# Optimization experiments

Hardware: AMD Instinct MI355X
Metric: run time of the kernel (lower is better)

## Reference

```python
import jax, jax.numpy as jnp
import numpy as np

B, S, D = 8, 1024, 1024
H, DK = 16, 64  # num_heads, d_k; H*DK == D
NEG_INF = 1e29


def setup_inputs() -> dict:
    key = jax.random.key(0)
    ks = jax.random.split(key, 12)
    sc = 1.0 / np.sqrt(D)
    q = jax.random.normal(ks[0], (B, S, D), jnp.float32)
    k = jax.random.normal(ks[1], (B, S, D), jnp.float32)
    v = jax.random.normal(ks[2], (B, S, D), jnp.float32)
    # causal mask, broadcast per batch (mask==0 positions are masked out)
    mask = jnp.broadcast_to(jnp.tril(jnp.ones((S, S), jnp.int32)), (B, S, S))
    Wq = jax.random.normal(ks[3], (D, D), jnp.float32) * sc
    bq = jax.random.normal(ks[4], (D,), jnp.float32) * 0.01
    Wk = jax.random.normal(ks[5], (D, D), jnp.float32) * sc
    bk = jax.random.normal(ks[6], (D,), jnp.float32) * 0.01
    Wv = jax.random.normal(ks[7], (D, D), jnp.float32) * sc
    bv = jax.random.normal(ks[8], (D,), jnp.float32) * 0.01
    Wo = jax.random.normal(ks[9], (D, D), jnp.float32) * sc
    bo = jax.random.normal(ks[10], (D,), jnp.float32) * 0.01
    return {"q": q, "k": k, "v": v, "mask": mask,
            "Wq": Wq, "bq": bq, "Wk": Wk, "bk": bk,
            "Wv": Wv, "bv": bv, "Wo": Wo, "bo": bo}


def reference(q, k, v, mask, Wq, bq, Wk, bk, Wv, bv, Wo, bo):
    # Linear projections (torch Linear: x @ W.T + b)
    q1 = q @ Wq.T + bq
    k1 = k @ Wk.T + bk
    v1 = v @ Wv.T + bv
    # [B, S, D] -> [B, H, S, DK]
    def split_heads(x):
        return x.reshape(B, S, H, DK).transpose(0, 2, 1, 3)
    q3, k3, v3 = split_heads(q1), split_heads(k1), split_heads(v1)
    # scores [B, H, S, S]
    scores = jnp.einsum('bhqd,bhkd->bhqk', q3, k3) / jnp.sqrt(jnp.float32(DK))
    scores = jnp.where(mask[:, None, :, :] == 0, -NEG_INF, scores)
    probs = jax.nn.softmax(scores, axis=-1)
    attn = jnp.einsum('bhqk,bhkd->bhqd', probs, v3)  # [B, H, S, DK]
    out = attn.transpose(0, 2, 1, 3).reshape(B, S, D)
    return out @ Wo.T + bo
```

## Files before the change

kernel.cpp:

```cpp
#include <hip/hip_runtime.h>
#include <hip/hip_bf16.h>
#include <stdint.h>

constexpr int NB = 8;
constexpr int NS = 1024;
constexpr int ND = 1024;
constexpr int NH = 16;
constexpr int NDK = 64;
constexpr int NT = NS / 64;

typedef __bf16 bf16_t;
typedef __attribute__((ext_vector_type(8))) __bf16 bf16x8;
typedef __attribute__((ext_vector_type(4))) __bf16 bf16x4;
typedef __attribute__((ext_vector_type(4))) float f32x4;

#define GLL16(g, s) __builtin_amdgcn_global_load_lds( \
    (const __attribute__((address_space(1))) void*)(g), \
    (__attribute__((address_space(3))) void*)(s), 16, 0, 0)

__device__ __forceinline__ void cvt_body(const float* __restrict__ s,
                                         bf16_t* __restrict__ d, long n) {
  long i0 = (long)(blockIdx.x * blockDim.x + threadIdx.x) * 4;
  long step = (long)gridDim.x * blockDim.x * 4;
  for (long i = i0; i < n; i += step) {
    float4 f = *(const float4*)(s + i);
    bf16x4 o;
    o[0] = (bf16_t)f.x; o[1] = (bf16_t)f.y; o[2] = (bf16_t)f.z; o[3] = (bf16_t)f.w;
    *(bf16x4*)(d + i) = o;
  }
}

__global__ __launch_bounds__(256) void cvt3_kernel(const float* s0, bf16_t* d0,
                                                   const float* s1, bf16_t* d1,
                                                   const float* s2, bf16_t* d2, long n) {
  const float* s = blockIdx.y == 0 ? s0 : blockIdx.y == 1 ? s1 : s2;
  bf16_t* d = blockIdx.y == 0 ? d0 : blockIdx.y == 1 ? d1 : d2;
  cvt_body(s, d, n);
}

__global__ __launch_bounds__(256) void cvt4_kernel(const float* s0, bf16_t* d0,
                                                   const float* s1, bf16_t* d1,
                                                   const float* s2, bf16_t* d2,
                                                   const float* s3, bf16_t* d3, long n) {
  const float* s = blockIdx.y == 0 ? s0 : blockIdx.y == 1 ? s1 : blockIdx.y == 2 ? s2 : s3;
  bf16_t* d = blockIdx.y == 0 ? d0 : blockIdx.y == 1 ? d1 : blockIdx.y == 2 ? d2 : d3;
  cvt_body(s, d, n);
}

template<bool OUT_F32>
__device__ __forceinline__ void gemm_body(bf16_t* S,
                                          const bf16_t* __restrict__ A,
                                          const bf16_t* __restrict__ W,
                                          const float* __restrict__ bias,
                                          void* __restrict__ Cout,
                                          int M, int N, int K, int bx, int by) {
  const int tid = threadIdx.x;
  const int l = tid & 63, w = tid >> 6;
  const int wr = w >> 1, wc = w & 1;
  const int g = l >> 4, r = l & 15;
  const int m0 = by * 256, n0 = bx * 128;
  const int wbase = w * 512;

  auto stageA2 = [&](int q, int t, int half) {
#pragma unroll
    for (int it = half * 2; it < half * 2 + 2; ++it) {
      int idx = it * 512 + tid;
      int row = idx >> 3, c = (idx & 7) ^ (row & 7);
      GLL16(A + (size_t)(m0 + row) * K + (t << 6) + c * 8,
            S + q * 24576 + it * 4096 + wbase);
    }
  };
  auto stageB2 = [&](int q, int t) {
#pragma unroll
    for (int it = 0; it < 2; ++it) {
      int idx = it * 512 + tid;
      int row = idx >> 3, c = (idx & 7) ^ (row & 7);
      GLL16(W + (size_t)(n0 + row) * K + (t << 6) + c * 8,
            S + q * 24576 + 16384 + it * 4096 + wbase);
    }
  };

  f32x4 acc[4][4] = {};
  const int NKT = K >> 6;

  stageA2(0, 0, 0); stageA2(0, 0, 1); stageB2(0, 0);
  stageA2(1, 1, 0); stageA2(1, 1, 1); stageB2(1, 1);

  int q = 0;
  for (int t = 0; t < NKT; ++t) {
    const bool pf = (t + 2 < NKT);
    int q2 = q + 2; if (q2 >= 3) q2 -= 3;

    if (t + 1 < NKT) asm volatile("s_waitcnt vmcnt(6)" ::: "memory");
    else             asm volatile("s_waitcnt vmcnt(0)" ::: "memory");
    __builtin_amdgcn_s_barrier();

    const bf16_t* a_ = S + q * 24576;
    const bf16_t* b_ = a_ + 16384;

#pragma unroll
    for (int kk = 0; kk < 2; ++kk) {
      bf16x8 bw[4];
#pragma unroll
      for (int n = 0; n < 4; ++n) {
        int row = wc * 64 + n * 16 + r;
        bw[n] = *(const bf16x8*)(b_ + row * 64 + (((kk * 4 + g) ^ (row & 7)) << 3));
      }
#pragma unroll
      for (int mh = 0; mh < 2; ++mh) {
        bf16x8 af[2];
#pragma unroll
        for (int i = 0; i < 2; ++i) {
          int row = wr * 64 + (mh * 2 + i) * 16 + r;
          af[i] = *(const bf16x8*)(a_ + row * 64 + (((kk * 4 + g) ^ (row & 7)) << 3));
        }
        if (pf) {
          int ph = kk * 2 + mh;
          if (ph == 0)      stageA2(q2, t + 2, 0);
          else if (ph == 1) stageA2(q2, t + 2, 1);
          else if (ph == 2) stageB2(q2, t + 2);
        }
        __builtin_amdgcn_s_barrier();
        asm volatile("s_waitcnt lgkmcnt(0)" ::: "memory");
        __builtin_amdgcn_sched_barrier(0);
        __builtin_amdgcn_s_setprio(1);
#pragma unroll
        for (int i = 0; i < 2; ++i)
#pragma unroll
          for (int n = 0; n < 4; ++n)
            acc[mh * 2 + i][n] = __builtin_amdgcn_mfma_f32_16x16x32_bf16(
                af[i], bw[n], acc[mh * 2 + i][n], 0, 0, 0);
        __builtin_amdgcn_s_setprio(0);
        __builtin_amdgcn_sched_barrier(0);
      }
    }
    ++q; if (q >= 3) q -= 3;
  }

#pragma unroll
  for (int n = 0; n < 4; ++n) {
    int col = n0 + wc * 64 + n * 16 + r;
    float bv = bias[col];
#pragma unroll
    for (int m = 0; m < 4; ++m) {
      int row0 = m0 + wr * 64 + m * 16 + g * 4;
#pragma unroll
      for (int j = 0; j < 4; ++j) {
        float vv = acc[m][n][j] + bv;
        if (OUT_F32)
          ((float*)Cout)[(size_t)(row0 + j) * N + col] = vv;
        else
          ((bf16_t*)Cout)[(size_t)(row0 + j) * N + col] = (bf16_t)vv;
      }
    }
  }
}

__global__ __launch_bounds__(512, 2) void gemm_bt(const bf16_t* __restrict__ A,
                                                  const bf16_t* __restrict__ W,
                                                  const float* __restrict__ bias,
                                                  float* __restrict__ Cout,
                                                  int M, int N, int K) {
  __shared__ bf16_t S[3 * 24576];
  const int o = blockIdx.x;
  const int xcd = o & 7, s = o >> 3;
  const int bx = s & 7, u = s >> 3;
  const int by = xcd + 8 * u;
  gemm_body<true>(S, A, W, bias, (void*)Cout, M, N, K, bx, by);
}

__global__ __launch_bounds__(512, 2) void gemm_qkv(
    const bf16_t* A0, const bf16_t* W0, const float* b0, bf16_t* C0,
    const bf16_t* A1, const bf16_t* W1, const float* b1, bf16_t* C1,
    const bf16_t* A2, const bf16_t* W2, const float* b2, bf16_t* C2,
    int M, int N, int K) {
  __shared__ bf16_t S[3 * 24576];
  const int o = blockIdx.x;
  const int xcd = o & 7, s = o >> 3;
  const int bx = s & 7, u = s >> 3;
  const int zby = xcd + 8 * u;
  const int z = zby >> 5, by = zby & 31;
  const bf16_t* A = z == 0 ? A0 : z == 1 ? A1 : A2;
  const bf16_t* W = z == 0 ? W0 : z == 1 ? W1 : W2;
  const float* bb = z == 0 ? b0 : z == 1 ? b1 : b2;
  bf16_t* C = z == 0 ? C0 : z == 1 ? C1 : C2;
  gemm_body<false>(S, A, W, bb, (void*)C, M, N, K, bx, by);
}

__global__ __launch_bounds__(256, 4) void attn_kernel(const bf16_t* __restrict__ Q1,
                                                      const bf16_t* __restrict__ K1,
                                                      const bf16_t* __restrict__ V1,
                                                      bf16_t* __restrict__ attn) {
  __shared__ bf16_t Kt[2][64 * 64];
  __shared__ bf16_t Vt[2][64 * 64];
  __shared__ bf16_t Pl[4][16 * 64];

  const int tid = threadIdx.x;
  const int l = tid & 63, w = tid >> 6;
  const int g = l >> 4, r = l & 15;

  const int o = blockIdx.x;
  const int os = (o & 7) * 128 + (o >> 3);
  const int pair = os & 7, hb = os >> 3;
  const int h = hb & 15, b = hb >> 4;

  constexpr float SC = 0.18033688011112042f;

  for (int ph = 0; ph < 2; ++ph) {
    const int qt = ph ? (NT - 1 - pair) : pair;
    const int qrow_g = qt * 64 + w * 16 + r;

    const bf16_t* qptr = Q1 + ((size_t)b * NS + qrow_g) * ND + h * 64;
    bf16x8 qf0 = *(const bf16x8*)(qptr + g * 8);
    bf16x8 qf1 = *(const bf16x8*)(qptr + 32 + g * 8);
#pragma unroll
    for (int i = 0; i < 8; ++i) {
      qf0[i] = (bf16_t)((float)qf0[i] * SC);
      qf1[i] = (bf16_t)((float)qf1[i] * SC);
    }

    float mrun = -1e30f, lrun = 0.f;
    f32x4 oacc[4] = {};

    __syncthreads();

    bf16x8 vr0, vr1;
    {
#pragma unroll
      for (int it = 0; it < 2; ++it) {
        int idx = it * 256 + tid;
        int key = idx >> 3;
        int dkg = ((idx & 7) ^ (key & 7)) << 3;
        GLL16(K1 + ((size_t)b * NS + key) * ND + h * 64 + dkg,
              &Kt[0][(it * 256 + w * 64) * 8]);
      }
      vr0 = *(const bf16x8*)(V1 + ((size_t)b * NS + l) * ND + h * 64 + w * 8);
      vr1 = *(const bf16x8*)(V1 + ((size_t)b * NS + l) * ND + h * 64 + (4 + w) * 8);
    }

    for (int kt = 0; kt <= qt; ++kt) {
      const int p = kt & 1;
      const int k0 = kt * 64;

#pragma unroll
      for (int it = 0; it < 2; ++it) {
        int dkb = (it * 4 + w) * 8;
#pragma unroll
        for (int jj = 0; jj < 8; ++jj) {
          int dk = dkb + jj;
          int boff = dk * 128 + ((l * 2) ^ ((dk & 7) << 4));
          *(bf16_t*)((char*)Vt[p] + boff) = (it ? vr1 : vr0)[jj];
        }
      }
      __syncthreads();

      if (kt < qt) {
        const int k0n = k0 + 64;
#pragma unroll
        for (int it = 0; it < 2; ++it) {
          int idx = it * 256 + tid;
          int key = idx >> 3;
          int dkg = ((idx & 7) ^ (key & 7)) << 3;
          GLL16(K1 + ((size_t)b * NS + k0n + key) * ND + h * 64 + dkg,
                &Kt[p ^ 1][(it * 256 + w * 64) * 8]);
        }
        vr0 = *(const bf16x8*)(V1 + ((size_t)b * NS + k0n + l) * ND + h * 64 + w * 8);
        vr1 = *(const bf16x8*)(V1 + ((size_t)b * NS + k0n + l) * ND + h * 64 + (4 + w) * 8);
      }

      f32x4 sacc[4] = {};
      __builtin_amdgcn_s_setprio(1);
#pragma unroll
      for (int n = 0; n < 4; ++n) {
        int key = n * 16 + r;
#pragma unroll
        for (int kk = 0; kk < 2; ++kk) {
          int dk2 = kk * 32 + g * 8;
          int boff = key * 128 + ((dk2 * 2) ^ ((key & 7) << 4));
          bf16x8 kf = *(const bf16x8*)((char*)Kt[p] + boff);
          sacc[n] = __builtin_amdgcn_mfma_f32_16x16x32_bf16(kf, kk == 0 ? qf0 : qf1, sacc[n], 0, 0, 0);
        }
      }
      __builtin_amdgcn_s_setprio(0);

      if (kt == qt) {
#pragma unroll
        for (int n = 0; n < 4; ++n)
#pragma unroll
          for (int j = 0; j < 4; ++j)
            if (k0 + n * 16 + g * 4 + j > qrow_g) sacc[n][j] = -1e30f;
      }

      float mx;
      {
        float t0 = fmaxf(fmaxf(sacc[0][0], sacc[0][1]), fmaxf(sacc[0][2], sacc[0][3]));
        float t1 = fmaxf(fmaxf(sacc[1][0], sacc[1][1]), fmaxf(sacc[1][2], sacc[1][3]));
        float t2 = fmaxf(fmaxf(sacc[2][0], sacc[2][1]), fmaxf(sacc[2][2], sacc[2][3]));
        float t3 = fmaxf(fmaxf(sacc[3][0], sacc[3][1]), fmaxf(sacc[3][2], sacc[3][3]));
        mx = fmaxf(fmaxf(t0, t1), fmaxf(t2, t3));
      }
      mx = fmaxf(mx, __shfl_xor(mx, 16));
      mx = fmaxf(mx, __shfl_xor(mx, 32));

      if (!__all(mx <= mrun + 8.0f)) {
        float m_new = fmaxf(mrun, mx);
        float esc = __builtin_amdgcn_exp2f(mrun - m_new);
        mrun = m_new;
        lrun *= esc;
#pragma unroll
        for (int n = 0; n < 4; ++n)
#pragma unroll
          for (int j = 0; j < 4; ++j) oacc[n][j] *= esc;
      }

      float rsum = 0.f;
#pragma unroll
      for (int n = 0; n < 4; ++n) {
        bf16x4 p4;
#pragma unroll
        for (int j = 0; j < 4; ++j) {
          float pe = __builtin_amdgcn_exp2f(sacc[n][j] - mrun);
          rsum += pe;
          p4[j] = (bf16_t)pe;
        }
        *(bf16x4*)((char*)Pl[w] + r * 128 + ((n * 32 + g * 8) ^ ((r & 7) << 4))) = p4;
      }
      rsum += __shfl_xor(rsum, 16);
      rsum += __shfl_xor(rsum, 32);
      lrun += rsum;

      __builtin_amdgcn_s_setprio(1);
#pragma unroll
      for (int kk = 0; kk < 2; ++kk) {
        bf16x8 pf = *(const bf16x8*)((char*)Pl[w] + r * 128 + ((kk * 64 + g * 16) ^ ((r & 7) << 4)));
#pragma unroll
        for (int n = 0; n < 4; ++n) {
          int dkr = n * 16 + r;
          bf16x8 vf = *(const bf16x8*)((char*)Vt[p] + dkr * 128 + ((kk * 64 + g * 16) ^ ((r & 7) << 4)));
          oacc[n] = __builtin_amdgcn_mfma_f32_16x16x32_bf16(vf, pf, oacc[n], 0, 0, 0);
        }
      }
      __builtin_amdgcn_s_setprio(0);
    }

    float linv = 1.0f / lrun;
#pragma unroll
    for (int n = 0; n < 4; ++n) {
      bf16x4 o4;
#pragma unroll
      for (int j = 0; j < 4; ++j) o4[j] = (bf16_t)(oacc[n][j] * linv);
      *(bf16x4*)(attn + ((size_t)b * NS + qrow_g) * ND + h * 64 + n * 16 + g * 4) = o4;
    }
  }
}

extern "C" void kernel_launch(void* const* d_in, const int* in_sizes, int n_in,
                              void* d_out, int out_size, void* d_ws, size_t ws_size,
                              hipStream_t stream) {
  const float* q  = (const float*)d_in[0];
  const float* k  = (const float*)d_in[1];
  const float* v  = (const float*)d_in[2];
  const float* Wq = (const float*)d_in[4];
  const float* bq = (const float*)d_in[5];
  const float* Wk = (const float*)d_in[6];
  const float* bk = (const float*)d_in[7];
  const float* Wv = (const float*)d_in[8];
  const float* bv = (const float*)d_in[9];
  const float* Wo = (const float*)d_in[10];
  const float* bo = (const float*)d_in[11];
  float* out = (float*)d_out;

  const size_t NX = (size_t)NB * NS * ND;
  const size_t NW = (size_t)ND * ND;
  char* ws = (char*)d_ws;
  size_t off = 0;
  auto alloc = [&](size_t bytes) {
    char* p = ws + off;
    off += (bytes + 255) & ~(size_t)255;
    return p;
  };
  bf16_t* xq  = (bf16_t*)alloc(NX * 2);
  bf16_t* xk  = (bf16_t*)alloc(NX * 2);
  bf16_t* xv  = (bf16_t*)alloc(NX * 2);
  bf16_t* wqb = (bf16_t*)alloc(NW * 2);
  bf16_t* wkb = (bf16_t*)alloc(NW * 2);
  bf16_t* wvb = (bf16_t*)alloc(NW * 2);
  bf16_t* wob = (bf16_t*)alloc(NW * 2);
  bf16_t* q1  = (bf16_t*)alloc(NX * 2);
  bf16_t* k1  = (bf16_t*)alloc(NX * 2);
  bf16_t* v1  = (bf16_t*)alloc(NX * 2);
  bf16_t* at  = xq;

  dim3 blk(256);
  cvt3_kernel<<<dim3(1024, 3), blk, 0, stream>>>(q, xq, k, xk, v, xv, (long)NX);
  cvt4_kernel<<<dim3(128, 4), blk, 0, stream>>>(Wq, wqb, Wk, wkb, Wv, wvb, Wo, wob, (long)NW);

  gemm_qkv<<<dim3(768), dim3(512), 0, stream>>>(
      xq, wqb, bq, q1, xk, wkb, bk, k1, xv, wvb, bv, v1, NB * NS, ND, ND);

  attn_kernel<<<dim3((NT / 2) * NH * NB), blk, 0, stream>>>(q1, k1, v1, at);

  gemm_bt<<<dim3(256), dim3(512), 0, stream>>>(at, wob, bo, out, NB * NS, ND, ND);
}
```

Measured before the change: 158.3 us.

## Fuse fp32-to-bf16 activation conversion into the QKV projection GEMM

Removes the separate cvt3 kernel that turned q/k/v into bf16 in a workspace buffer. The QKV GEMM now reads fp32 activations straight into registers, converts them to bf16 and writes them into a double-buffered swizzled LDS tile, while weights still use async global-to-LDS loads in a triple buffer. This avoids writing and rereading about 48MB of bf16 activations and one kernel launch. In exchange the A-tile loads go through registers, which costs register pressure and VGPR-mediated LDS writes, and the pipeline now has a single barrier per k-step.

```diff
diff --git a/kernel.cpp b/kernel.cpp
--- a/kernel.cpp
+++ b/kernel.cpp
@@ -8,6 +8,7 @@
 constexpr int NH = 16;
 constexpr int NDK = 64;
 constexpr int NT = NS / 64;
+constexpr int NKT = ND / 64;
 
 typedef __bf16 bf16_t;
 typedef __attribute__((ext_vector_type(8))) __bf16 bf16x8;
@@ -30,14 +31,6 @@
   }
 }
 
-__global__ __launch_bounds__(256) void cvt3_kernel(const float* s0, bf16_t* d0,
-                                                   const float* s1, bf16_t* d1,
-                                                   const float* s2, bf16_t* d2, long n) {
-  const float* s = blockIdx.y == 0 ? s0 : blockIdx.y == 1 ? s1 : s2;
-  bf16_t* d = blockIdx.y == 0 ? d0 : blockIdx.y == 1 ? d1 : d2;
-  cvt_body(s, d, n);
-}
-
 __global__ __launch_bounds__(256) void cvt4_kernel(const float* s0, bf16_t* d0,
                                                    const float* s1, bf16_t* d1,
                                                    const float* s2, bf16_t* d2,
@@ -47,13 +40,21 @@
   cvt_body(s, d, n);
 }
 
-template<bool OUT_F32>
-__device__ __forceinline__ void gemm_body(bf16_t* S,
-                                          const bf16_t* __restrict__ A,
-                                          const bf16_t* __restrict__ W,
-                                          const float* __restrict__ bias,
-                                          void* __restrict__ Cout,
-                                          int M, int N, int K, int bx, int by) {
+__global__ __launch_bounds__(512, 2) void gemm_qkv(
+    const float* A0, const bf16_t* W0, const float* b0, bf16_t* C0,
+    const float* A1, const bf16_t* W1, const float* b1, bf16_t* C1,
+    const float* A2, const bf16_t* W2, const float* b2, bf16_t* C2) {
+  __shared__ bf16_t S[2 * 16384 + 3 * 8192];
+  const int o = blockIdx.x;
+  const int xcd = o & 7, s = o >> 3;
+  const int bx = s & 7, u = s >> 3;
+  const int zby = xcd + 8 * u;
+  const int z = zby >> 5, by = zby & 31;
+  const float* A = z == 0 ? A0 : z == 1 ? A1 : A2;
+  const bf16_t* W = z == 0 ? W0 : z == 1 ? W1 : W2;
+  const float* bb = z == 0 ? b0 : z == 1 ? b1 : b2;
+  bf16_t* C = z == 0 ? C0 : z == 1 ? C1 : C2;
+
   const int tid = threadIdx.x;
   const int l = tid & 63, w = tid >> 6;
   const int wr = w >> 1, wc = w & 1;
@@ -61,97 +62,101 @@
   const int m0 = by * 256, n0 = bx * 128;
   const int wbase = w * 512;
 
-  auto stageA2 = [&](int q, int t, int half) {
-#pragma unroll
-    for (int it = half * 2; it < half * 2 + 2; ++it) {
-      int idx = it * 512 + tid;
-      int row = idx >> 3, c = (idx & 7) ^ (row & 7);
-      GLL16(A + (size_t)(m0 + row) * K + (t << 6) + c * 8,
-            S + q * 24576 + it * 4096 + wbase);
-    }
-  };
-  auto stageB2 = [&](int q, int t) {
+  bf16_t* Ab = S;
+  bf16_t* Bb = S + 32768;
+
+  float4 fa[8];
+  auto issueA = [&](int t) {
+#pragma unroll
+    for (int it = 0; it < 4; ++it) {
+      const float* p = A + (size_t)(m0 + it * 64 + (tid >> 3)) * ND + t * 64 + (tid & 7) * 8;
+      fa[it * 2]     = *(const float4*)p;
+      fa[it * 2 + 1] = *(const float4*)(p + 4);
+    }
+  };
+  auto writeA = [&](int ab) {
+#pragma unroll
+    for (int it = 0; it < 4; ++it) {
+      int row = it * 64 + (tid >> 3), c = tid & 7;
+      bf16x8 ov;
+      ov[0] = (bf16_t)fa[it * 2].x;     ov[1] = (bf16_t)fa[it * 2].y;
+      ov[2] = (bf16_t)fa[it * 2].z;     ov[3] = (bf16_t)fa[it * 2].w;
+      ov[4] = (bf16_t)fa[it * 2 + 1].x; ov[5] = (bf16_t)fa[it * 2 + 1].y;
+      ov[6] = (bf16_t)fa[it * 2 + 1].z; ov[7] = (bf16_t)fa[it * 2 + 1].w;
+      *(bf16x8*)(Ab + ab * 16384 + row * 64 + ((c ^ (row & 7)) << 3)) = ov;
+    }
+  };
+  auto stageB = [&](int qb, int t) {
 #pragma unroll
     for (int it = 0; it < 2; ++it) {
       int idx = it * 512 + tid;
       int row = idx >> 3, c = (idx & 7) ^ (row & 7);
-      GLL16(W + (size_t)(n0 + row) * K + (t << 6) + c * 8,
-            S + q * 24576 + 16384 + it * 4096 + wbase);
+      GLL16(W + (size_t)(n0 + row) * ND + (t << 6) + c * 8,
+            Bb + qb * 8192 + it * 4096 + wbase);
     }
   };
 
   f32x4 acc[4][4] = {};
-  const int NKT = K >> 6;
-
-  stageA2(0, 0, 0); stageA2(0, 0, 1); stageB2(0, 0);
-  stageA2(1, 1, 0); stageA2(1, 1, 1); stageB2(1, 1);
-
-  int q = 0;
+
+  issueA(0);
+  stageB(0, 0);
+  stageB(1, 1);
+  asm volatile("s_waitcnt vmcnt(0)" ::: "memory");
+  __builtin_amdgcn_sched_barrier(0);
+  writeA(0);
+  asm volatile("s_waitcnt lgkmcnt(0)" ::: "memory");
+  __builtin_amdgcn_s_barrier();
+
   for (int t = 0; t < NKT; ++t) {
-    const bool pf = (t + 2 < NKT);
-    int q2 = q + 2; if (q2 >= 3) q2 -= 3;
-
-    if (t + 1 < NKT) asm volatile("s_waitcnt vmcnt(6)" ::: "memory");
-    else             asm volatile("s_waitcnt vmcnt(0)" ::: "memory");
-    __builtin_amdgcn_s_barrier();
-
-    const bf16_t* a_ = S + q * 24576;
-    const bf16_t* b_ = a_ + 16384;
-
+    if (t + 1 < NKT) issueA(t + 1);
+    __builtin_amdgcn_sched_barrier(0);
+    if (t + 2 < NKT) stageB((t + 2) % 3, t + 2);
+    __builtin_amdgcn_sched_barrier(0);
+
+    const bf16_t* a_ = Ab + (t & 1) * 16384;
+    const bf16_t* b_ = Bb + (t % 3) * 8192;
 #pragma unroll
     for (int kk = 0; kk < 2; ++kk) {
-      bf16x8 bw[4];
+      bf16x8 af[4], bw[4];
+#pragma unroll
+      for (int m = 0; m < 4; ++m) {
+        int row = wr * 64 + m * 16 + r;
+        af[m] = *(const bf16x8*)(a_ + row * 64 + (((kk * 4 + g) ^ (row & 7)) << 3));
+      }
 #pragma unroll
       for (int n = 0; n < 4; ++n) {
         int row = wc * 64 + n * 16 + r;
         bw[n] = *(const bf16x8*)(b_ + row * 64 + (((kk * 4 + g) ^ (row & 7)) << 3));
       }
-#pragma unroll
-      for (int mh = 0; mh < 2; ++mh) {
-        bf16x8 af[2];
-#pragma unroll
-        for (int i = 0; i < 2; ++i) {
-          int row = wr * 64 + (mh * 2 + i) * 16 + r;
-          af[i] = *(const bf16x8*)(a_ + row * 64 + (((kk * 4 + g) ^ (row & 7)) << 3));
-        }
-        if (pf) {
-          int ph = kk * 2 + mh;
-          if (ph == 0)      stageA2(q2, t + 2, 0);
-          else if (ph == 1) stageA2(q2, t + 2, 1);
-          else if (ph == 2) stageB2(q2, t + 2);
-        }
-        __builtin_amdgcn_s_barrier();
-        asm volatile("s_waitcnt lgkmcnt(0)" ::: "memory");
-        __builtin_amdgcn_sched_barrier(0);
-        __builtin_amdgcn_s_setprio(1);
-#pragma unroll
-        for (int i = 0; i < 2; ++i)
-#pragma unroll
-          for (int n = 0; n < 4; ++n)
-            acc[mh * 2 + i][n] = __builtin_amdgcn_mfma_f32_16x16x32_bf16(
-                af[i], bw[n], acc[mh * 2 + i][n], 0, 0, 0);
-        __builtin_amdgcn_s_setprio(0);
-        __builtin_amdgcn_sched_barrier(0);
-      }
-    }
-    ++q; if (q >= 3) q -= 3;
+      __builtin_amdgcn_s_setprio(1);
+#pragma unroll
+      for (int m = 0; m < 4; ++m)
+#pragma unroll
+        for (int n = 0; n < 4; ++n)
+          acc[m][n] = __builtin_amdgcn_mfma_f32_16x16x32_bf16(af[m], bw[n], acc[m][n], 0, 0, 0);
+      __builtin_amdgcn_s_setprio(0);
+    }
+
+    if (t + 1 < NKT) {
+      if (t + 2 < NKT) asm volatile("s_waitcnt vmcnt(2)" ::: "memory");
+      else             asm volatile("s_waitcnt vmcnt(0)" ::: "memory");
+      __builtin_amdgcn_sched_barrier(0);
+      writeA((t + 1) & 1);
+    }
+    asm volatile("s_waitcnt lgkmcnt(0)" ::: "memory");
+    __builtin_amdgcn_s_barrier();
   }
 
 #pragma unroll
   for (int n = 0; n < 4; ++n) {
     int col = n0 + wc * 64 + n * 16 + r;
-    float bv = bias[col];
+    float bv = bb[col];
 #pragma unroll
     for (int m = 0; m < 4; ++m) {
       int row0 = m0 + wr * 64 + m * 16 + g * 4;
 #pragma unroll
-      for (int j = 0; j < 4; ++j) {
-        float vv = acc[m][n][j] + bv;
-        if (OUT_F32)
-          ((float*)Cout)[(size_t)(row0 + j) * N + col] = vv;
-        else
-          ((bf16_t*)Cout)[(size_t)(row0 + j) * N + col] = (bf16_t)vv;
-      }
+      for (int j = 0; j < 4; ++j)
+        C[(size_t)(row0 + j) * ND + col] = (bf16_t)(acc[m][n][j] + bv);
     }
   }
 }
@@ -166,25 +171,102 @@
   const int xcd = o & 7, s = o >> 3;
   const int bx = s & 7, u = s >> 3;
   const int by = xcd + 8 * u;
-  gemm_body<true>(S, A, W, bias, (void*)Cout, M, N, K, bx, by);
-}
-
-__global__ __launch_bounds__(512, 2) void gemm_qkv(
-    const bf16_t* A0, const bf16_t* W0, const float* b0, bf16_t* C0,
-    const bf16_t* A1, const bf16_t* W1, const float* b1, bf16_t* C1,
-    const bf16_t* A2, const bf16_t* W2, const float* b2, bf16_t* C2,
-    int M, int N, int K) {
-  __shared__ bf16_t S[3 * 24576];
-  const int o = blockIdx.x;
-  const int xcd = o & 7, s = o >> 3;
-  const int bx = s & 7, u = s >> 3;
-  const int zby = xcd + 8 * u;
-  const int z = zby >> 5, by = zby & 31;
-  const bf16_t* A = z == 0 ? A0 : z == 1 ? A1 : A2;
-  const bf16_t* W = z == 0 ? W0 : z == 1 ? W1 : W2;
-  const float* bb = z == 0 ? b0 : z == 1 ? b1 : b2;
-  bf16_t* C = z == 0 ? C0 : z == 1 ? C1 : C2;
-  gemm_body<false>(S, A, W, bb, (void*)C, M, N, K, bx, by);
+
+  const int tid = threadIdx.x;
+  const int l = tid & 63, w = tid >> 6;
+  const int wr = w >> 1, wc = w & 1;
+  const int g = l >> 4, r = l & 15;
+  const int m0 = by * 256, n0 = bx * 128;
+  const int wbase = w * 512;
+
+  auto stageA2 = [&](int q, int t, int half) {
+#pragma unroll
+    for (int it = half * 2; it < half * 2 + 2; ++it) {
+      int idx = it * 512 + tid;
+      int row = idx >> 3, c = (idx & 7) ^ (row & 7);
+      GLL16(A + (size_t)(m0 + row) * K + (t << 6) + c * 8,
+            S + q * 24576 + it * 4096 + wbase);
+    }
+  };
+  auto stageB2 = [&](int q, int t) {
+#pragma unroll
+    for (int it = 0; it < 2; ++it) {
+      int idx = it * 512 + tid;
+      int row = idx >> 3, c = (idx & 7) ^ (row & 7);
+      GLL16(W + (size_t)(n0 + row) * K + (t << 6) + c * 8,
+            S + q * 24576 + 16384 + it * 4096 + wbase);
+    }
+  };
+
+  f32x4 acc[4][4] = {};
+  const int NKT2 = K >> 6;
+
+  stageA2(0, 0, 0); stageA2(0, 0, 1); stageB2(0, 0);
+  stageA2(1, 1, 0); stageA2(1, 1, 1); stageB2(1, 1);
+
+  int q = 0;
+  for (int t = 0; t < NKT2; ++t) {
+    const bool pf = (t + 2 < NKT2);
+    int q2 = q + 2; if (q2 >= 3) q2 -= 3;
+
+    if (t + 1 < NKT2) asm volatile("s_waitcnt vmcnt(6)" ::: "memory");
+    else              asm volatile("s_waitcnt vmcnt(0)" ::: "memory");
+    __builtin_amdgcn_s_barrier();
+
+    const bf16_t* a_ = S + q * 24576;
+    const bf16_t* b_ = a_ + 16384;
+
+#pragma unroll
+    for (int kk = 0; kk < 2; ++kk) {
+      bf16x8 bw[4];
+#pragma unroll
+      for (int n = 0; n < 4; ++n) {
+        int row = wc * 64 + n * 16 + r;
+        bw[n] = *(const bf16x8*)(b_ + row * 64 + (((kk * 4 + g) ^ (row & 7)) << 3));
+      }
+#pragma unroll
+      for (int mh = 0; mh < 2; ++mh) {
+        bf16x8 af[2];
+#pragma unroll
+        for (int i = 0; i < 2; ++i) {
+          int row = wr * 64 + (mh * 2 + i) * 16 + r;
+          af[i] = *(const bf16x8*)(a_ + row * 64 + (((kk * 4 + g) ^ (row & 7)) << 3));
+        }
+        if (pf) {
+          int ph = kk * 2 + mh;
+          if (ph == 0)      stageA2(q2, t + 2, 0);
+          else if (ph == 1) stageA2(q2, t + 2, 1);
+          else if (ph == 2) stageB2(q2, t + 2);
+        }
+        __builtin_amdgcn_s_barrier();
+        asm volatile("s_waitcnt lgkmcnt(0)" ::: "memory");
+        __builtin_amdgcn_sched_barrier(0);
+        __builtin_amdgcn_s_setprio(1);
+#pragma unroll
+        for (int i = 0; i < 2; ++i)
+#pragma unroll
+          for (int n = 0; n < 4; ++n)
+            acc[mh * 2 + i][n] = __builtin_amdgcn_mfma_f32_16x16x32_bf16(
+                af[i], bw[n], acc[mh * 2 + i][n], 0, 0, 0);
+        __builtin_amdgcn_s_setprio(0);
+        __builtin_amdgcn_sched_barrier(0);
+      }
+    }
+    ++q; if (q >= 3) q -= 3;
+  }
+
+#pragma unroll
+  for (int n = 0; n < 4; ++n) {
+    int col = n0 + wc * 64 + n * 16 + r;
+    float bv = bias[col];
+#pragma unroll
+    for (int m = 0; m < 4; ++m) {
+      int row0 = m0 + wr * 64 + m * 16 + g * 4;
+#pragma unroll
+      for (int j = 0; j < 4; ++j)
+        Cout[(size_t)(row0 + j) * N + col] = acc[m][n][j] + bv;
+    }
+  }
 }
 
 __global__ __launch_bounds__(256, 4) void attn_kernel(const bf16_t* __restrict__ Q1,
@@ -379,9 +461,6 @@
     off += (bytes + 255) & ~(size_t)255;
     return p;
   };
-  bf16_t* xq  = (bf16_t*)alloc(NX * 2);
-  bf16_t* xk  = (bf16_t*)alloc(NX * 2);
-  bf16_t* xv  = (bf16_t*)alloc(NX * 2);
   bf16_t* wqb = (bf16_t*)alloc(NW * 2);
   bf16_t* wkb = (bf16_t*)alloc(NW * 2);
   bf16_t* wvb = (bf16_t*)alloc(NW * 2);
@@ -389,14 +468,13 @@
   bf16_t* q1  = (bf16_t*)alloc(NX * 2);
   bf16_t* k1  = (bf16_t*)alloc(NX * 2);
   bf16_t* v1  = (bf16_t*)alloc(NX * 2);
-  bf16_t* at  = xq;
+  bf16_t* at  = (bf16_t*)alloc(NX * 2);
 
   dim3 blk(256);
-  cvt3_kernel<<<dim3(1024, 3), blk, 0, stream>>>(q, xq, k, xk, v, xv, (long)NX);
   cvt4_kernel<<<dim3(128, 4), blk, 0, stream>>>(Wq, wqb, Wk, wkb, Wv, wvb, Wo, wob, (long)NW);
 
   gemm_qkv<<<dim3(768), dim3(512), 0, stream>>>(
-      xq, wqb, bq, q1, xk, wkb, bk, k1, xv, wvb, bv, v1, NB * NS, ND, ND);
+      q, wqb, bq, q1, k, wkb, bk, k1, v, wvb, bv, v1);
 
   attn_kernel<<<dim3((NT / 2) * NH * NB), blk, 0, stream>>>(q1, k1, v1, at);
 
```

Result: faster. 148.4 us (-6.3%).
